# Optimization experiments

Hardware: AMD Instinct MI355X
Metric: run time of the kernel (lower is better)

Reference implementation:

```python
import jax, jax.numpy as jnp
import numpy as np
jax.config.update("jax_enable_x64", True)  # hash uses int64 like torch .long()

N_LEVELS = 16
F = 16
B = 1.38
BASE_RES = 16
T_PRIME = 1048583  # nextprime(2**20)
PS = np.array([1, 19349663, 83492791], dtype=np.int64)
BBOX = np.array([[-2., -2., -2.], [2., 2., 2.]], dtype=np.float32)
ENTRIES_NUM = np.array([int(BASE_RES * B ** i) for i in range(N_LEVELS)], dtype=np.int64)
ENTRIES_CNT = ENTRIES_NUM ** 3
ENTRIES_SIZE = (1.0 / (ENTRIES_NUM - 1)).astype(np.float32)
ENTRIES_SUM = np.cumsum(ENTRIES_CNT)
START_HASH = int(np.argmax(ENTRIES_CNT > T_PRIME))  # = 6
DENSE_TOTAL = int(ENTRIES_SUM[START_HASH - 1])      # = 822944
OFFSETS = np.array([[0,0,0],[0,0,1],[0,1,0],[0,1,1],[1,0,0],[1,0,1],[1,1,0],[1,1,1]], dtype=np.float32)

def setup_inputs() -> dict:
    key = jax.random.key(0)
    k1, k2, k3 = jax.random.split(key, 3)
    N = 65536
    xyz = jax.random.uniform(k1, (N, 3), dtype=jnp.float32, minval=-2.0, maxval=2.0)
    # kaiming_normal_ on a (L, T, F) tensor: fan_in = T*F, gain = sqrt(2)
    std = float(np.sqrt(2.0 / (T_PRIME * F)))
    dense = jax.random.normal(k2, (DENSE_TOTAL, F), dtype=jnp.float32) * std
    hash_table = jax.random.normal(k3, (N_LEVELS - START_HASH, T_PRIME, F), dtype=jnp.float32) * std
    return {"xyz": xyz, "dense": dense, "hash_table": hash_table}

def reference(xyz, dense, hash_table):
    bash = xyz.shape
    x = xyz.reshape(-1, 3)
    lo = jnp.asarray(BBOX[0]); hi = jnp.asarray(BBOX[1])
    xn = (x - lo) / (hi - lo)                                  # [N,3] in [0,1]
    es = jnp.asarray(ENTRIES_SIZE)                             # [L]
    num = jnp.asarray(ENTRIES_NUM)                             # [L] int64
    offs = jnp.asarray(OFFSETS)                                # [8,3]
    flt = xn[None] / es[:, None, None]                         # [L,N,3]
    int_xyz = (flt[:, :, None] + offs[None, None]).astype(jnp.int64)  # [L,N,8,3]
    int_xyz = jnp.clip(int_xyz, 0, (num - 1)[:, None, None, None])
    off = flt - int_xyz[:, :, 0].astype(flt.dtype)             # [L,N,3]
    S = START_HASH; H = N_LEVELS - S
    nS = num[:S][:, None, None]
    ind_dense = int_xyz[:S, ..., 0] * nS * nS + int_xyz[:S, ..., 1] * nS + int_xyz[:S, ..., 2]
    dense_off = jnp.concatenate([jnp.zeros((1,), jnp.int64), jnp.asarray(ENTRIES_SUM[:S - 1])])
    ind_dense = ind_dense + dense_off[:, None, None]           # [S,N,8]
    ih = int_xyz[S:]
    ind_hash = ((ih[..., 0] * PS[0]) ^ (ih[..., 1] * PS[1]) ^ (ih[..., 2] * PS[2])) % T_PRIME  # [H,N,8]
    val_dense = dense[ind_dense]                               # [S,N,8,F]
    val_hash = hash_table[jnp.arange(H)[:, None, None], ind_hash]  # [H,N,8,F]
    val = jnp.concatenate([val_dense, val_hash], axis=0)       # [L,N,8,F]
    mul = 1.0 - offs[None, None] + (2.0 * offs[None, None] - 1.0) * off[:, :, None]  # [L,N,8,3]
    w = mul[..., 0] * mul[..., 1]  # NOTE: original code omits the z weight; faithful
    val = (w[..., None] * val).sum(axis=-2)                    # [L,N,F]
    val = jnp.transpose(val, (1, 0, 2))                        # [N,L,F]
    val = val.sum(axis=-1)                                     # [N,L] sum_over_features
    out = jnp.concatenate([xn, val], axis=-1)                  # [N,3+L]
    return out.reshape(*bash[:-1], out.shape[-1])
```

## Files before the change

### kernel.cpp

```cpp
#include <hip/hip_runtime.h>


#define HE_T_PRIME 1048583ULL

static __device__ __constant__ int c_num[16] = {
    16, 22, 30, 42, 58, 80, 110, 152, 210, 290, 400, 553, 763, 1053, 1453, 2005};
static __device__ __constant__ float c_es[16] = {
    (float)(1.0 / 15.0),   (float)(1.0 / 21.0),   (float)(1.0 / 29.0),
    (float)(1.0 / 41.0),   (float)(1.0 / 57.0),   (float)(1.0 / 79.0),
    (float)(1.0 / 109.0),  (float)(1.0 / 151.0),  (float)(1.0 / 209.0),
    (float)(1.0 / 289.0),  (float)(1.0 / 399.0),  (float)(1.0 / 552.0),
    (float)(1.0 / 762.0),  (float)(1.0 / 1052.0), (float)(1.0 / 1452.0),
    (float)(1.0 / 2004.0)};
static __device__ __constant__ int c_doff[6] = {0, 4096, 14744, 41744, 115832, 310944};

__global__ __launch_bounds__(256) void HashEncoding_721554506107_kernel(
    const float* __restrict__ xyz, const float* __restrict__ dense,
    const float* __restrict__ hasht, float* __restrict__ out, int npts) {
  int tid = blockIdx.x * blockDim.x + threadIdx.x;
  int p = tid >> 4;
  if (p >= npts) return;
  int l = tid & 15;

  float px = xyz[3 * p + 0];
  float py = xyz[3 * p + 1];
  float pz = xyz[3 * p + 2];
  float xn0 = (px + 2.0f) * 0.25f;
  float xn1 = (py + 2.0f) * 0.25f;
  float xn2 = (pz + 2.0f) * 0.25f;
  if (l < 3) out[19 * p + l] = (l == 0) ? xn0 : ((l == 1) ? xn1 : xn2);

  int n = c_num[l];
  float es = c_es[l];
  float fx = xn0 / es;
  float fy = xn1 / es;
  float fz = xn2 / es;
  int nm1 = n - 1;
  int ix0 = min(max((int)fx, 0), nm1);
  int iy0 = min(max((int)fy, 0), nm1);
  int iz0 = min(max((int)fz, 0), nm1);
  int ix1 = min(max((int)(fx + 1.0f), 0), nm1);
  int iy1 = min(max((int)(fy + 1.0f), 0), nm1);
  int iz1 = min(max((int)(fz + 1.0f), 0), nm1);

  float ox = fx - (float)ix0;
  float oy = fy - (float)iy0;
  float wx[2] = {1.0f - ox, ox};
  float wy[2] = {1.0f - oy, oy};

  size_t idx[8];
  const float* tab;
  if (l < 6) {
    tab = dense;
    long long nn = (long long)n * (long long)n;
    long long doff = (long long)c_doff[l];
    long long ix[2] = {ix0, ix1};
    long long iy[2] = {iy0, iy1};
    long long iz[2] = {iz0, iz1};
#pragma unroll
    for (int c = 0; c < 8; ++c) {
      long long ind = ix[(c >> 2) & 1] * nn + iy[(c >> 1) & 1] * (long long)n +
                      iz[c & 1] + doff;
      idx[c] = (size_t)ind;
    }
  } else {
    tab = hasht + (size_t)(l - 6) * (size_t)(HE_T_PRIME * 16ULL);
    unsigned long long hx[2] = {(unsigned long long)ix0,
                                (unsigned long long)ix1};
    unsigned long long hy[2] = {(unsigned long long)iy0 * 19349663ULL,
                                (unsigned long long)iy1 * 19349663ULL};
    unsigned long long hz[2] = {(unsigned long long)iz0 * 83492791ULL,
                                (unsigned long long)iz1 * 83492791ULL};
#pragma unroll
    for (int c = 0; c < 8; ++c) {
      unsigned long long h = hx[(c >> 2) & 1] ^ hy[(c >> 1) & 1] ^ hz[c & 1];
      idx[c] = (size_t)(h % HE_T_PRIME);
    }
  }

  float acc = 0.0f;
#pragma unroll
  for (int c = 0; c < 8; ++c) {
    const float4* e = (const float4*)(tab + idx[c] * 16);
    float4 a = e[0];
    float4 b = e[1];
    float4 d = e[2];
    float4 g = e[3];
    float s = ((a.x + a.y) + (a.z + a.w)) + ((b.x + b.y) + (b.z + b.w)) +
              ((d.x + d.y) + (d.z + d.w)) + ((g.x + g.y) + (g.z + g.w));
    float w = wx[(c >> 2) & 1] * wy[(c >> 1) & 1];
    acc = fmaf(w, s, acc);
  }
  out[19 * p + 3 + l] = acc;
}

extern "C" void kernel_launch(void* const* d_in, const int* in_sizes, int n_in,
                              void* d_out, int out_size, void* d_ws,
                              size_t ws_size, hipStream_t stream) {
  const float* xyz = (const float*)d_in[0];
  const float* dense = (const float*)d_in[1];
  const float* hasht = (const float*)d_in[2];
  float* out = (float*)d_out;
  int npts = in_sizes[0] / 3;
  int total = npts * 16;
  int block = 256;
  int grid = (total + block - 1) / block;
  HashEncoding_721554506107_kernel<<<grid, block, 0, stream>>>(xyz, dense, hasht,
                                                               out, npts);
}
```

Measured before the change: 138.3 us.

## Split each table row across 4 lanes and make level a grid dimension

```diff
diff --git a/kernel.cpp b/kernel.cpp
--- a/kernel.cpp
+++ b/kernel.cpp
@@ -2,6 +2,7 @@
 
 
 #define HE_T_PRIME 1048583ULL
+typedef unsigned long long ull;
 
 static __device__ __constant__ int c_num[16] = {
     16, 22, 30, 42, 58, 80, 110, 152, 210, 290, 400, 553, 763, 1053, 1453, 2005};
@@ -17,81 +18,71 @@
 __global__ __launch_bounds__(256) void HashEncoding_721554506107_kernel(
     const float* __restrict__ xyz, const float* __restrict__ dense,
     const float* __restrict__ hasht, float* __restrict__ out, int npts) {
-  int tid = blockIdx.x * blockDim.x + threadIdx.x;
-  int p = tid >> 4;
+  const int l = blockIdx.y;
+  const int p = blockIdx.x * 64 + (threadIdx.x >> 2);
+  const int q = threadIdx.x & 3;
   if (p >= npts) return;
-  int l = tid & 15;
 
-  float px = xyz[3 * p + 0];
-  float py = xyz[3 * p + 1];
-  float pz = xyz[3 * p + 2];
-  float xn0 = (px + 2.0f) * 0.25f;
-  float xn1 = (py + 2.0f) * 0.25f;
-  float xn2 = (pz + 2.0f) * 0.25f;
-  if (l < 3) out[19 * p + l] = (l == 0) ? xn0 : ((l == 1) ? xn1 : xn2);
+  const float px = xyz[3 * p + 0];
+  const float py = xyz[3 * p + 1];
+  const float pz = xyz[3 * p + 2];
+  const float xn0 = (px + 2.0f) * 0.25f;
+  const float xn1 = (py + 2.0f) * 0.25f;
+  const float xn2 = (pz + 2.0f) * 0.25f;
+  if (l == 0 && q < 3) out[19 * p + q] = (q == 0) ? xn0 : ((q == 1) ? xn1 : xn2);
 
-  int n = c_num[l];
-  float es = c_es[l];
-  float fx = xn0 / es;
-  float fy = xn1 / es;
-  float fz = xn2 / es;
-  int nm1 = n - 1;
-  int ix0 = min(max((int)fx, 0), nm1);
-  int iy0 = min(max((int)fy, 0), nm1);
-  int iz0 = min(max((int)fz, 0), nm1);
-  int ix1 = min(max((int)(fx + 1.0f), 0), nm1);
-  int iy1 = min(max((int)(fy + 1.0f), 0), nm1);
-  int iz1 = min(max((int)(fz + 1.0f), 0), nm1);
+  const int n = c_num[l];
+  const float es = c_es[l];
+  const float fx = xn0 / es;
+  const float fy = xn1 / es;
+  const float fz = xn2 / es;
+  const int nm1 = n - 1;
+  const int ix0 = min(max((int)fx, 0), nm1);
+  const int iy0 = min(max((int)fy, 0), nm1);
+  const int iz0 = min(max((int)fz, 0), nm1);
+  const int ix1 = min(max((int)(fx + 1.0f), 0), nm1);
+  const int iy1 = min(max((int)(fy + 1.0f), 0), nm1);
+  const int iz1 = min(max((int)(fz + 1.0f), 0), nm1);
 
-  float ox = fx - (float)ix0;
-  float oy = fy - (float)iy0;
-  float wx[2] = {1.0f - ox, ox};
-  float wy[2] = {1.0f - oy, oy};
+  const float ox = fx - (float)ix0;
+  const float oy = fy - (float)iy0;
+  float wxy[4];
+  wxy[0] = (1.0f - ox) * (1.0f - oy);
+  wxy[1] = (1.0f - ox) * oy;
+  wxy[2] = ox * (1.0f - oy);
+  wxy[3] = ox * oy;
 
-  size_t idx[8];
-  const float* tab;
+  float acc = 0.0f;
   if (l < 6) {
-    tab = dense;
-    long long nn = (long long)n * (long long)n;
-    long long doff = (long long)c_doff[l];
-    long long ix[2] = {ix0, ix1};
-    long long iy[2] = {iy0, iy1};
-    long long iz[2] = {iz0, iz1};
+    const int nn = n * n;
+    const int base = c_doff[l];
+    const int ixs[2] = {ix0 * nn, ix1 * nn};
+    const int iys[2] = {iy0 * n, iy1 * n};
+    const int izs[2] = {iz0, iz1};
 #pragma unroll
     for (int c = 0; c < 8; ++c) {
-      long long ind = ix[(c >> 2) & 1] * nn + iy[(c >> 1) & 1] * (long long)n +
-                      iz[c & 1] + doff;
-      idx[c] = (size_t)ind;
+      const int ind = base + ixs[c >> 2] + iys[(c >> 1) & 1] + izs[c & 1];
+      const float4 v =
+          *(const float4*)(dense + (size_t)ind * 16 + (size_t)(q * 4));
+      acc = fmaf(wxy[c >> 1], (v.x + v.y) + (v.z + v.w), acc);
     }
   } else {
-    tab = hasht + (size_t)(l - 6) * (size_t)(HE_T_PRIME * 16ULL);
-    unsigned long long hx[2] = {(unsigned long long)ix0,
-                                (unsigned long long)ix1};
-    unsigned long long hy[2] = {(unsigned long long)iy0 * 19349663ULL,
-                                (unsigned long long)iy1 * 19349663ULL};
-    unsigned long long hz[2] = {(unsigned long long)iz0 * 83492791ULL,
-                                (unsigned long long)iz1 * 83492791ULL};
+    const float* tab = hasht + (size_t)(l - 6) * (size_t)(HE_T_PRIME * 16ULL);
+    const ull hx[2] = {(ull)ix0, (ull)ix1};
+    const ull hy[2] = {(ull)iy0 * 19349663ULL, (ull)iy1 * 19349663ULL};
+    const ull hz[2] = {(ull)iz0 * 83492791ULL, (ull)iz1 * 83492791ULL};
 #pragma unroll
     for (int c = 0; c < 8; ++c) {
-      unsigned long long h = hx[(c >> 2) & 1] ^ hy[(c >> 1) & 1] ^ hz[c & 1];
-      idx[c] = (size_t)(h % HE_T_PRIME);
+      const ull h = hx[c >> 2] ^ hy[(c >> 1) & 1] ^ hz[c & 1];
+      const size_t ind = (size_t)(h % HE_T_PRIME);
+      const float4 v = *(const float4*)(tab + ind * 16 + (size_t)(q * 4));
+      acc = fmaf(wxy[c >> 1], (v.x + v.y) + (v.z + v.w), acc);
     }
   }
 
-  float acc = 0.0f;
-#pragma unroll
-  for (int c = 0; c < 8; ++c) {
-    const float4* e = (const float4*)(tab + idx[c] * 16);
-    float4 a = e[0];
-    float4 b = e[1];
-    float4 d = e[2];
-    float4 g = e[3];
-    float s = ((a.x + a.y) + (a.z + a.w)) + ((b.x + b.y) + (b.z + b.w)) +
-              ((d.x + d.y) + (d.z + d.w)) + ((g.x + g.y) + (g.z + g.w));
-    float w = wx[(c >> 2) & 1] * wy[(c >> 1) & 1];
-    acc = fmaf(w, s, acc);
-  }
-  out[19 * p + 3 + l] = acc;
+  acc += __shfl_xor(acc, 1);
+  acc += __shfl_xor(acc, 2);
+  if (q == 0) out[19 * p + 3 + l] = acc;
 }
 
 extern "C" void kernel_launch(void* const* d_in, const int* in_sizes, int n_in,
@@ -101,10 +92,8 @@
   const float* dense = (const float*)d_in[1];
   const float* hasht = (const float*)d_in[2];
   float* out = (float*)d_out;
-  int npts = in_sizes[0] / 3;
-  int total = npts * 16;
-  int block = 256;
-  int grid = (total + block - 1) / block;
-  HashEncoding_721554506107_kernel<<<grid, block, 0, stream>>>(xyz, dense, hasht,
-                                                               out, npts);
+  const int npts = in_sizes[0] / 3;
+  dim3 grid((npts + 63) / 64, 16);
+  HashEncoding_721554506107_kernel<<<grid, 256, 0, stream>>>(xyz, dense, hasht,
+                                                             out, npts);
 }
```

Result: faster. 117.7 us (-14.9%).
